# Kernel optimization log

Hardware: AMD Instinct MI355X
Metric: run time of the kernel (lower is better)

The kernel has to match this reference:

```python
import jax, jax.numpy as jnp
import numpy as np

B, S, H, KV, D, HID = 1, 2048, 32, 8, 128, 4096
SCALE = D ** -0.5
EPS = 1e-5
QMAX = 127.0  # 8-bit symmetric fake quant


def fake_quant(x):
    # per-tensor symmetric int8 fake quantization with straight-through estimator
    s = jnp.maximum(jnp.max(jnp.abs(x)), 1e-5) / QMAX
    q = jnp.clip(jnp.round(x / s), -QMAX - 1.0, QMAX) * s
    return x + jax.lax.stop_gradient(q - x)


def rms_norm(x, w):
    xf = x.astype(jnp.float32)
    var = jnp.mean(xf * xf, axis=-1, keepdims=True)
    return (xf * jax.lax.rsqrt(var + EPS)).astype(x.dtype) * w


def rotate_half(x):
    h = x.shape[-1] // 2
    return jnp.concatenate([-x[..., h:], x[..., :h]], axis=-1)


def qlinear(x, W):
    # QuantLinear: fake-quant activation and weight, then matmul (no bias)
    return fake_quant(x) @ fake_quant(W).T


def setup_inputs() -> dict:
    key = jax.random.key(0)
    ks = jax.random.split(key, 5)
    hidden_states = jax.random.normal(ks[0], (B, S, HID), jnp.float32)
    # RoPE tables
    inv_freq = 1.0 / (10000.0 ** (np.arange(0, D, 2, dtype=np.float32) / D))
    freqs = np.outer(np.arange(S, dtype=np.float32), inv_freq)  # [S, D/2]
    emb = np.concatenate([freqs, freqs], axis=-1)  # [S, D]
    cos = jnp.asarray(np.cos(emb))[None]  # [1,S,D]
    sin = jnp.asarray(np.sin(emb))[None]
    # causal additive mask [1,1,S,S]
    mask = jnp.where(np.tril(np.ones((S, S), dtype=bool)), 0.0, -1e9).astype(jnp.float32)[None, None]
    Wq = jax.random.normal(ks[1], (H * D, HID), jnp.float32) * 0.02
    Wk = jax.random.normal(ks[2], (KV * D, HID), jnp.float32) * 0.02
    Wv = jax.random.normal(ks[3], (KV * D, HID), jnp.float32) * 0.02
    Wo = jax.random.normal(ks[4], (HID, H * D), jnp.float32) * 0.02
    q_norm_w = jnp.ones((D,), jnp.float32)
    k_norm_w = jnp.ones((D,), jnp.float32)
    return dict(hidden_states=hidden_states, cos=cos, sin=sin, attention_mask=mask,
                Wq=Wq, Wk=Wk, Wv=Wv, Wo=Wo, q_norm_w=q_norm_w, k_norm_w=k_norm_w)


def reference(hidden_states, cos, sin, attention_mask, Wq, Wk, Wv, Wo, q_norm_w, k_norm_w):
    b, s, _ = hidden_states.shape
    q = qlinear(hidden_states, Wq).reshape(b, s, H, D).transpose(0, 2, 1, 3)   # [B,H,S,D]
    k = qlinear(hidden_states, Wk).reshape(b, s, KV, D).transpose(0, 2, 1, 3)  # [B,KV,S,D]
    v = qlinear(hidden_states, Wv).reshape(b, s, KV, D).transpose(0, 2, 1, 3)
    q = rms_norm(q, q_norm_w)
    k = rms_norm(k, k_norm_w)
    c = cos[:, None]  # unsqueeze head dim -> [1,1,S,D]
    sn = sin[:, None]
    q = q * c + rotate_half(q) * sn
    k = k * c + rotate_half(k) * sn
    n_rep = H // KV
    k = jnp.repeat(k, n_rep, axis=1)  # [B,H,S,D]
    v = jnp.repeat(v, n_rep, axis=1)
    # fake-quant around QK^T
    q = fake_quant(q)
    k = fake_quant(k)
    scores = jnp.einsum('bhqd,bhkd->bhqk', q, k) * SCALE + attention_mask
    p = jax.nn.softmax(scores.astype(jnp.float32), axis=-1).astype(q.dtype)
    # fake-quant around PV
    p = fake_quant(p)
    v = fake_quant(v)
    out = jnp.einsum('bhqk,bhkd->bhqd', p, v)
    out = out.transpose(0, 2, 1, 3).reshape(b, s, H * D)
    return qlinear(out, Wo)
```

## Files before the change

### kernel.cpp

```cpp
#include <hip/hip_runtime.h>
#include <hip/hip_bf16.h>
#include <math.h>
#include <stdint.h>

#define S_LEN 2048
#define NH    32
#define NKV   8
#define HD    128
#define HIDD  4096

typedef unsigned short u16;
typedef __attribute__((ext_vector_type(4))) int i32x4;

#define GLD16(g, l) __builtin_amdgcn_global_load_lds( \
    (const __attribute__((address_space(1))) void*)(g), \
    (__attribute__((address_space(3))) void*)(l), 16, 0, 0)


__device__ __forceinline__ float slot_scale(const unsigned* slot) {
    return fmaxf(__uint_as_float(*slot), 1e-5f) / 127.0f;
}

__device__ __forceinline__ float exp2_fast(float x) {
    float r; asm("v_exp_f32 %0, %1" : "=v"(r) : "v"(x)); return r;
}

__device__ __forceinline__ int qint(float x, float s) {
    float q = rintf(x / s);
    q = fminf(fmaxf(q, -128.0f), 127.0f);
    return (int)q;
}

__device__ __forceinline__ void block_amax_atomic(float m, unsigned* slot) {
    __shared__ float wmax[8];
    const int lane = threadIdx.x & 63;
    const int wid  = threadIdx.x >> 6;
    const int nw   = blockDim.x >> 6;
    #pragma unroll
    for (int o = 32; o; o >>= 1) m = fmaxf(m, __shfl_xor(m, o));
    if (lane == 0) wmax[wid] = m;
    __syncthreads();
    if (threadIdx.x == 0) {
        float bm = wmax[0];
        for (int i = 1; i < nw; ++i) bm = fmaxf(bm, wmax[i]);
        atomicMax(slot, __float_as_uint(bm));
    }
}

struct Amax5Args { const float* p[5]; size_t n4[5]; };
__global__ __launch_bounds__(256) void absmax5_kernel(Amax5Args a, unsigned* slots) {
    const int t = blockIdx.y;
    const float4* x4 = (const float4*)a.p[t];
    const size_t n4 = a.n4[t];
    size_t i = (size_t)blockIdx.x * blockDim.x + threadIdx.x;
    size_t stride = (size_t)gridDim.x * blockDim.x;
    float m = 0.0f;
    for (; i < n4; i += stride) {
        float4 v = x4[i];
        m = fmaxf(m, fmaxf(fmaxf(fabsf(v.x), fabsf(v.y)), fmaxf(fabsf(v.z), fabsf(v.w))));
    }
    block_amax_atomic(m, slots + t);
}

struct Quant5Args { const float* p[5]; char* o[5]; size_t n4[5]; };
__global__ __launch_bounds__(256) void quant5_kernel(Quant5Args a, const unsigned* slots) {
    const int t = blockIdx.y;
    float s = slot_scale(slots + t);
    const float4* x4 = (const float4*)a.p[t];
    unsigned* o4 = (unsigned*)a.o[t];
    const size_t n4 = a.n4[t];
    size_t i = (size_t)blockIdx.x * blockDim.x + threadIdx.x;
    size_t stride = (size_t)gridDim.x * blockDim.x;
    for (; i < n4; i += stride) {
        float4 v = x4[i];
        unsigned o = (unsigned)(qint(v.x, s) & 255)
                   | ((unsigned)(qint(v.y, s) & 255) << 8)
                   | ((unsigned)(qint(v.z, s) & 255) << 16)
                   | ((unsigned)(qint(v.w, s) & 255) << 24);
        o4[i] = o;
    }
}

__global__ __launch_bounds__(256) void quant_kernel(const float* __restrict__ x,
                                                    size_t n4, const unsigned* slot,
                                                    char* __restrict__ out) {
    float s = slot_scale(slot);
    size_t i = (size_t)blockIdx.x * blockDim.x + threadIdx.x;
    size_t stride = (size_t)gridDim.x * blockDim.x;
    const float4* x4 = (const float4*)x;
    unsigned* o4 = (unsigned*)out;
    for (; i < n4; i += stride) {
        float4 v = x4[i];
        unsigned o = (unsigned)(qint(v.x, s) & 255)
                   | ((unsigned)(qint(v.y, s) & 255) << 8)
                   | ((unsigned)(qint(v.z, s) & 255) << 16)
                   | ((unsigned)(qint(v.w, s) & 255) << 24);
        o4[i] = o;
    }
}

__device__ __forceinline__ void gemm_body(const char* __restrict__ A,
                                          const char* __restrict__ B,
                                          float* __restrict__ C,
                                          int m0, int n0, int N, int K,
                                          float scale, unsigned* out_amax,
                                          char* Asm, char* Bsm) {
    const int tid  = threadIdx.x;
    const int lane = tid & 63;
    const int wave = tid >> 6;
    const int wr = (wave >> 1) * 64;
    const int wc = (wave & 1) * 64;
    const int l15 = lane & 15;
    const int l4  = lane >> 4;
    const int cx  = (l4 ^ (l15 & 3)) * 16;
    const int r0  = tid >> 2;
    const int sc  = ((tid & 3) ^ ((tid >> 2) & 3)) * 16;

    i32x4 acc[4][4];
    #pragma unroll
    for (int i = 0; i < 4; ++i)
        #pragma unroll
        for (int j = 0; j < 4; ++j) acc[i][j] = (i32x4){0, 0, 0, 0};

    auto STAGE = [&](int buf, int k0) {
        GLD16(&A[(size_t)(m0 + r0) * K + k0 + sc],      &Asm[buf * 8192 + wave * 1024]);
        GLD16(&A[(size_t)(m0 + 64 + r0) * K + k0 + sc], &Asm[buf * 8192 + 4096 + wave * 1024]);
        GLD16(&B[(size_t)(n0 + r0) * K + k0 + sc],      &Bsm[buf * 8192 + wave * 1024]);
        GLD16(&B[(size_t)(n0 + 64 + r0) * K + k0 + sc], &Bsm[buf * 8192 + 4096 + wave * 1024]);
    };

    STAGE(0, 0);
    __syncthreads();
    int cur = 0;
    const int NT = K >> 6;
    for (int t = 0; t < NT; ++t) {
        if (t + 1 < NT) STAGE(cur ^ 1, (t + 1) << 6);
        i32x4 af[4], bfr[4];
        #pragma unroll
        for (int i = 0; i < 4; ++i)
            af[i] = *(const i32x4*)&Asm[cur * 8192 + (wr + i * 16 + l15) * 64 + cx];
        #pragma unroll
        for (int j = 0; j < 4; ++j)
            bfr[j] = *(const i32x4*)&Bsm[cur * 8192 + (wc + j * 16 + l15) * 64 + cx];
        #pragma unroll
        for (int i = 0; i < 4; ++i)
            #pragma unroll
            for (int j = 0; j < 4; ++j)
                acc[i][j] = __builtin_amdgcn_mfma_i32_16x16x64_i8(af[i], bfr[j], acc[i][j], 0, 0, 0);
        __syncthreads();
        cur ^= 1;
    }

    float lm = 0.0f;
    #pragma unroll
    for (int i = 0; i < 4; ++i)
        #pragma unroll
        for (int j = 0; j < 4; ++j)
            #pragma unroll
            for (int r = 0; r < 4; ++r) {
                int row = m0 + wr + i * 16 + l4 * 4 + r;
                int col = n0 + wc + j * 16 + l15;
                float v = (float)acc[i][j][r] * scale;
                C[(size_t)row * N + col] = v;
                lm = fmaxf(lm, fabsf(v));
            }
    if (out_amax) block_amax_atomic(lm, out_amax);
}

__global__ __launch_bounds__(256) void gemm_qkv_kernel(const char* __restrict__ Aq,
                                                       const char* __restrict__ Wqq,
                                                       const char* __restrict__ Wkq,
                                                       const char* __restrict__ Wvq,
                                                       float* __restrict__ qf,
                                                       float* __restrict__ kf,
                                                       float* __restrict__ vf,
                                                       const unsigned* __restrict__ slots,
                                                       unsigned* v_amax) {
    __shared__ __align__(16) char Asm[2 * 8192];
    __shared__ __align__(16) char Bsm[2 * 8192];
    int bid = blockIdx.x;
    int swz = (bid & 7) * 96 + (bid >> 3);
    int x = swz & 15, y = swz >> 4;
    const char* B; float* C; int N, nb; const unsigned* sB; unsigned* am = nullptr;
    if (y < 32)      { B = Wqq; C = qf; N = NH * HD;  nb = y;      sB = slots + 1; }
    else if (y < 40) { B = Wkq; C = kf; N = NKV * HD; nb = y - 32; sB = slots + 2; }
    else             { B = Wvq; C = vf; N = NKV * HD; nb = y - 40; sB = slots + 3; am = v_amax; }
    float scale = slot_scale(slots + 0) * slot_scale(sB);
    gemm_body(Aq, B, C, x * 128, nb * 128, N, HIDD, scale, am, Asm, Bsm);
}

__global__ __launch_bounds__(256) void gemm_o_kernel(const char* __restrict__ A,
                                                     const char* __restrict__ Woq,
                                                     float* __restrict__ C,
                                                     const unsigned* __restrict__ slots) {
    __shared__ __align__(16) char Asm[2 * 8192];
    __shared__ __align__(16) char Bsm[2 * 8192];
    int bid = blockIdx.x;
    int swz = (bid & 7) * 64 + (bid >> 3);
    int x = swz & 15, y = swz >> 4;
    float scale = slot_scale(slots + 8) * slot_scale(slots + 4);
    gemm_body(A, Woq, C, x * 128, y * 128, NH * HD, HIDD, scale, nullptr, Asm, Bsm);
}

__global__ __launch_bounds__(256) void rmsrope2_kernel(float* __restrict__ qx,
                                                       float* __restrict__ kx,
                                                       const float* __restrict__ cosb,
                                                       const float* __restrict__ sinb,
                                                       const float* __restrict__ qw,
                                                       const float* __restrict__ kw,
                                                       unsigned* slots) {
    const int which = blockIdx.y;
    float* x = which ? kx : qx;
    const float* w = which ? kw : qw;
    const int s_shift = which ? 3 : 5;
    const int nrows = which ? (S_LEN * NKV) : (S_LEN * NH);
    unsigned* slot = slots + (which ? 6 : 5);

    const int lane = threadIdx.x & 63;
    const int wid  = threadIdx.x >> 6;
    const float wa = w[lane];
    const float wb = w[lane + 64];
    float lm = 0.0f;
    for (int row = blockIdx.x * 4 + wid; row < nrows; row += gridDim.x * 4) {
        int s = row >> s_shift;
        float* xr = x + (size_t)row * 128;
        float a = xr[lane], b = xr[lane + 64];
        float ss = a * a + b * b;
        #pragma unroll
        for (int o = 32; o; o >>= 1) ss += __shfl_xor(ss, o);
        float inv = 1.0f / sqrtf(ss * (1.0f / 128.0f) + 1e-5f);
        float ya = (a * inv) * wa;
        float yb = (b * inv) * wb;
        const float* cr = cosb + (size_t)s * 128;
        const float* sr = sinb + (size_t)s * 128;
        float o0 = ya * cr[lane]      - yb * sr[lane];
        float o1 = yb * cr[lane + 64] + ya * sr[lane + 64];
        xr[lane] = o0;
        xr[lane + 64] = o1;
        lm = fmaxf(lm, fmaxf(fabsf(o0), fabsf(o1)));
    }
    block_amax_atomic(lm, slot);
}

__global__ __launch_bounds__(256) void quant_qk2_kernel(const float* __restrict__ qx,
                                                        const float* __restrict__ kx,
                                                        const unsigned* slots,
                                                        char* __restrict__ qq,
                                                        char* __restrict__ kq) {
    int tid = blockIdx.x * 256 + threadIdx.x;
    const int qtot = S_LEN * NH * HD;
    if (tid < qtot) {
        float s = slot_scale(slots + 5);
        int d  = tid & 127;
        int h  = (tid >> 7) & 31;
        int sp = tid >> 12;
        qq[((size_t)h * S_LEN + sp) * 128 + d] = (char)qint(qx[tid], s);
    } else {
        tid -= qtot;
        float s = slot_scale(slots + 6);
        int d  = tid & 127;
        int h  = (tid >> 7) & 7;
        int sp = tid >> 10;
        kq[((size_t)h * S_LEN + sp) * 128 + d] = (char)qint(kx[tid], s);
    }
}

__global__ __launch_bounds__(256) void quant_v_kernel(const float* __restrict__ x,
                                                      const unsigned* slot,
                                                      char* __restrict__ out) {
    __shared__ unsigned char t8[64][36];
    const float s = slot_scale(slot);
    const int t   = threadIdx.x;
    const int sp0 = blockIdx.x * 64;
    const int d0  = blockIdx.y * 32;
    const int kvh = blockIdx.z;
    const int dl = t & 31;
    const int sb = t >> 5;
    #pragma unroll
    for (int j = 0; j < 8; ++j) {
        int spl = sb + j * 8;
        float v = x[((size_t)(sp0 + spl) * NKV + kvh) * 128 + d0 + dl];
        t8[spl][dl] = (unsigned char)qint(v, s);
    }
    __syncthreads();
    const int dd = t >> 3;
    const int ch = t & 7;
    unsigned lo = 0, hi = 0;
    #pragma unroll
    for (int j = 0; j < 4; ++j) lo |= (unsigned)t8[ch * 8 + j][dd] << (8 * j);
    #pragma unroll
    for (int j = 0; j < 4; ++j) hi |= (unsigned)t8[ch * 8 + 4 + j][dd] << (8 * j);
    *(uint2*)&out[((size_t)kvh * 128 + d0 + dd) * S_LEN + sp0 + ch * 8] = make_uint2(lo, hi);
}

__global__ __launch_bounds__(256) void attn_kernel(const char* __restrict__ Qq,
                                                   const char* __restrict__ Kq,
                                                   const char* __restrict__ Vt,
                                                   const unsigned* sq_slot,
                                                   const unsigned* sk_slot,
                                                   const unsigned* sv_slot,
                                                   float* __restrict__ O,
                                                   unsigned* amax_slot) {
    __shared__ __align__(16) char Klds[64 * 144];
    __shared__ __align__(16) char Vlds[128 * 80];
    __shared__ __align__(16) char plds[4][16 * 80];

    const int tid  = threadIdx.x;
    const int lane = tid & 63;
    const int wave = tid >> 6;
    const int h  = blockIdx.y;
    const int kv = h >> 2;
    const int l15 = lane & 15;
    const int l4  = lane >> 4;
    const size_t kvS = (size_t)kv * S_LEN;

    const float sq = slot_scale(sq_slot);
    const float sk = slot_scale(sk_slot);
    const float sv = slot_scale(sv_slot);
    const float qs2 = sq * sk * 0.08838834764831845f * 1.4426950408889634f;
    const float osc = (1.0f / 127.0f) * sv;
    const float NEG = -1e30f;

    float lm = 0.0f;

    #pragma unroll 1
    for (int tpass = 0; tpass < 2; ++tpass) {
        const int qt  = tpass ? (31 - (int)blockIdx.x) : (int)blockIdx.x;
        const int qr0 = qt * 64 + wave * 16;
        const int nchunk = qt + 1;

        i32x4 qf2[2];
        {
            const char* qp = Qq + ((size_t)h * S_LEN + qr0 + l15) * 128 + l4 * 16;
            qf2[0] = *(const i32x4*)(qp);
            qf2[1] = *(const i32x4*)(qp + 64);
        }

        float m_l = NEG, l_l = 0.0f;

        auto qk_block = [&](int hb) -> i32x4 {
            i32x4 sacc = {0, 0, 0, 0};
            #pragma unroll
            for (int c = 0; c < 2; ++c) {
                i32x4 kfa = *(const i32x4*)&Klds[(hb * 16 + l15) * 144 + c * 64 + l4 * 16];
                sacc = __builtin_amdgcn_mfma_i32_16x16x64_i8(kfa, qf2[c], sacc, 0, 0, 0);
            }
            return sacc;
        };
        auto p1_interior = [&](int hb) {
            i32x4 sacc = qk_block(hb);
            float x0 = (float)sacc[0] * qs2, x1 = (float)sacc[1] * qs2;
            float x2 = (float)sacc[2] * qs2, x3 = (float)sacc[3] * qs2;
            float bm = fmaxf(fmaxf(x0, x1), fmaxf(x2, x3));
            float mn = fmaxf(m_l, bm);
            float ps = exp2_fast(x0 - mn) + exp2_fast(x1 - mn)
                     + exp2_fast(x2 - mn) + exp2_fast(x3 - mn);
            l_l = l_l * exp2_fast(m_l - mn) + ps;
            m_l = mn;
        };
        auto p1_diag = [&](int hb) {
            i32x4 sacc = qk_block(hb);
            float x[4];
            #pragma unroll
            for (int r = 0; r < 4; ++r) {
                float v = (float)sacc[r] * qs2;
                x[r] = ((l4 * 4 + r) > l15) ? NEG : v;
            }
            float bm = fmaxf(fmaxf(x[0], x[1]), fmaxf(x[2], x[3]));
            float mn = fmaxf(m_l, bm);
            float ps = exp2_fast(x[0] - mn) + exp2_fast(x[1] - mn)
                     + exp2_fast(x[2] - mn) + exp2_fast(x[3] - mn);
            l_l = l_l * exp2_fast(m_l - mn) + ps;
            m_l = mn;
        };

        i32x4 kreg[2];
        #pragma unroll
        for (int c = 0; c < 2; ++c) {
            int idx = c * 256 + tid;
            kreg[c] = *(const i32x4*)&Kq[(kvS + (idx >> 3)) * 128 + (idx & 7) * 16];
        }
        #pragma unroll 1
        for (int kc = 0; kc < nchunk; ++kc) {
            __syncthreads();
            #pragma unroll
            for (int c = 0; c < 2; ++c) {
                int idx = c * 256 + tid;
                *(i32x4*)&Klds[(idx >> 3) * 144 + (idx & 7) * 16] = kreg[c];
            }
            __syncthreads();
            if (kc + 1 < nchunk) {
                #pragma unroll
                for (int c = 0; c < 2; ++c) {
                    int idx = c * 256 + tid;
                    kreg[c] = *(const i32x4*)&Kq[(kvS + (kc + 1) * 64 + (idx >> 3)) * 128 + (idx & 7) * 16];
                }
            }
            if (kc < qt) {
                p1_interior(0); p1_interior(1); p1_interior(2); p1_interior(3);
            } else {
                #pragma unroll
                for (int hb = 0; hb < 4; ++hb) {
                    if (hb < wave) p1_interior(hb);
                    else if (hb == wave) p1_diag(hb);
                }
            }
        }
        float m2 = fmaxf(m_l, __shfl_xor(m_l, 16));
        float mfin = fmaxf(m2, __shfl_xor(m2, 32));
        float t = l_l * exp2_fast(m_l - mfin);
        t += __shfl_xor(t, 16);
        t += __shfl_xor(t, 32);
        float rl = 127.0f / t;

        i32x4 oacc[8];
        #pragma unroll
        for (int dt = 0; dt < 8; ++dt) oacc[dt] = (i32x4){0, 0, 0, 0};

        auto p2_interior = [&](int hb) -> unsigned {
            i32x4 sacc = qk_block(hb);
            unsigned pack = 0;
            #pragma unroll
            for (int r = 0; r < 4; ++r) {
                float x = (float)sacc[r] * qs2;
                float pq = rintf(exp2_fast(x - mfin) * rl);
                pack |= ((unsigned)(int)pq) << (8 * r);
            }
            return pack;
        };
        auto p2_diag = [&](int hb) -> unsigned {
            i32x4 sacc = qk_block(hb);
            unsigned pack = 0;
            #pragma unroll
            for (int r = 0; r < 4; ++r) {
                float x = (float)sacc[r] * qs2;
                float p = exp2_fast(x - mfin) * rl;
                float pq = ((l4 * 4 + r) > l15) ? 0.0f : rintf(p);
                pack |= ((unsigned)(int)pq) << (8 * r);
            }
            return pack;
        };

        i32x4 vreg[2];
        #pragma unroll
        for (int c = 0; c < 2; ++c) {
            int idx = c * 256 + tid;
            kreg[c] = *(const i32x4*)&Kq[(kvS + (idx >> 3)) * 128 + (idx & 7) * 16];
            vreg[c] = *(const i32x4*)&Vt[((size_t)kv * 128 + (idx >> 2)) * S_LEN + (idx & 3) * 16];
        }
        #pragma unroll 1
        for (int kc = 0; kc < nchunk; ++kc) {
            __syncthreads();
            #pragma unroll
            for (int c = 0; c < 2; ++c) {
                int idx = c * 256 + tid;
                *(i32x4*)&Klds[(idx >> 3) * 144 + (idx & 7) * 16] = kreg[c];
                *(i32x4*)&Vlds[(idx >> 2) * 80 + (idx & 3) * 16] = vreg[c];
            }
            __syncthreads();
            if (kc + 1 < nchunk) {
                #pragma unroll
                for (int c = 0; c < 2; ++c) {
                    int idx = c * 256 + tid;
                    kreg[c] = *(const i32x4*)&Kq[(kvS + (kc + 1) * 64 + (idx >> 3)) * 128 + (idx & 7) * 16];
                    vreg[c] = *(const i32x4*)&Vt[((size_t)kv * 128 + (idx >> 2)) * S_LEN + (kc + 1) * 64 + (idx & 3) * 16];
                }
            }
            if (kc < qt) {
                #pragma unroll
                for (int hb = 0; hb < 4; ++hb)
                    *(unsigned*)&plds[wave][l15 * 80 + hb * 16 + l4 * 4] = p2_interior(hb);
            } else {
                #pragma unroll
                for (int hb = 0; hb < 4; ++hb) {
                    unsigned pack = 0;
                    if (hb < wave) pack = p2_interior(hb);
                    else if (hb == wave) pack = p2_diag(hb);
                    *(unsigned*)&plds[wave][l15 * 80 + hb * 16 + l4 * 4] = pack;
                }
            }
            i32x4 pf = *(const i32x4*)&plds[wave][l15 * 80 + l4 * 16];
            #pragma unroll
            for (int dt = 0; dt < 8; ++dt) {
                i32x4 vfb = *(const i32x4*)&Vlds[(dt * 16 + l15) * 80 + l4 * 16];
                oacc[dt] = __builtin_amdgcn_mfma_i32_16x16x64_i8(pf, vfb, oacc[dt], 0, 0, 0);
            }
        }

        #pragma unroll
        for (int dt = 0; dt < 8; ++dt)
            #pragma unroll
            for (int r = 0; r < 4; ++r) {
                int qrow = qr0 + l4 * 4 + r;
                float v = (float)oacc[dt][r] * osc;
                O[(size_t)qrow * (NH * 128) + h * 128 + dt * 16 + l15] = v;
                lm = fmaxf(lm, fabsf(v));
            }
    }
    block_amax_atomic(lm, amax_slot);
}

extern "C" void kernel_launch(void* const* d_in, const int* in_sizes, int n_in,
                              void* d_out, int out_size, void* d_ws, size_t ws_size,
                              hipStream_t stream) {
    const float* hs   = (const float*)d_in[0];
    const float* cosb = (const float*)d_in[1];
    const float* sinb = (const float*)d_in[2];
    const float* Wq   = (const float*)d_in[4];
    const float* Wk   = (const float*)d_in[5];
    const float* Wv   = (const float*)d_in[6];
    const float* Wo   = (const float*)d_in[7];
    const float* qnw  = (const float*)d_in[8];
    const float* knw  = (const float*)d_in[9];
    float* out = (float*)d_out;

    char* ws = (char*)d_ws;
    unsigned* slots = (unsigned*)ws;
    size_t off = 256;
    auto take = [&](size_t bytes) { size_t o = off; off += (bytes + 255) & ~(size_t)255; return o; };
    char*  hsq  = (char*)(ws + take((size_t)S_LEN * HIDD));
    char*  Wqq  = (char*)(ws + take((size_t)NH * HD * HIDD));
    char*  Wkq  = (char*)(ws + take((size_t)NKV * HD * HIDD));
    char*  Wvq  = (char*)(ws + take((size_t)NKV * HD * HIDD));
    char*  Woq  = (char*)(ws + take((size_t)HIDD * NH * HD));
    float* qf   = (float*)(ws + take((size_t)S_LEN * NH * HD * 4));
    float* kf   = (float*)(ws + take((size_t)S_LEN * NKV * HD * 4));
    float* vf   = (float*)(ws + take((size_t)S_LEN * NKV * HD * 4));
    char*  qq   = (char*)(ws + take((size_t)NH * S_LEN * HD));
    char*  kq   = (char*)(ws + take((size_t)NKV * S_LEN * HD));
    char*  vtq  = (char*)(ws + take((size_t)NKV * HD * S_LEN));
    float* attnf = qf;
    char*  attnq = hsq;

    hipMemsetAsync(ws, 0, 64, stream);

    const size_t n_hs = (size_t)S_LEN * HIDD;
    const size_t n_wq = (size_t)NH * HD * HIDD;
    const size_t n_wk = (size_t)NKV * HD * HIDD;

    Amax5Args aa;
    aa.p[0] = hs; aa.p[1] = Wq; aa.p[2] = Wk; aa.p[3] = Wv; aa.p[4] = Wo;
    aa.n4[0] = n_hs / 4; aa.n4[1] = n_wq / 4; aa.n4[2] = n_wk / 4;
    aa.n4[3] = n_wk / 4; aa.n4[4] = n_wq / 4;
    absmax5_kernel<<<dim3(512, 5), 256, 0, stream>>>(aa, slots);

    Quant5Args qa;
    qa.p[0] = hs; qa.p[1] = Wq; qa.p[2] = Wk; qa.p[3] = Wv; qa.p[4] = Wo;
    qa.o[0] = hsq; qa.o[1] = Wqq; qa.o[2] = Wkq; qa.o[3] = Wvq; qa.o[4] = Woq;
    qa.n4[0] = n_hs / 4; qa.n4[1] = n_wq / 4; qa.n4[2] = n_wk / 4;
    qa.n4[3] = n_wk / 4; qa.n4[4] = n_wq / 4;
    quant5_kernel<<<dim3(1024, 5), 256, 0, stream>>>(qa, slots);

    gemm_qkv_kernel<<<768, 256, 0, stream>>>(hsq, Wqq, Wkq, Wvq, qf, kf, vf,
                                             slots, slots + 7);

    rmsrope2_kernel<<<dim3(1024, 2), 256, 0, stream>>>(qf, kf, cosb, sinb, qnw, knw, slots);

    quant_qk2_kernel<<<40960, 256, 0, stream>>>(qf, kf, slots, qq, kq);
    quant_v_kernel<<<dim3(32, 4, 8), 256, 0, stream>>>(vf, slots + 7, vtq);

    attn_kernel<<<dim3(16, NH), 256, 0, stream>>>(qq, kq, vtq,
                                                  slots + 5, slots + 6, slots + 7,
                                                  attnf, slots + 8);

    quant_kernel<<<2048, 256, 0, stream>>>(attnf, n_hs / 4, slots + 8, attnq);
    gemm_o_kernel<<<512, 256, 0, stream>>>(attnq, Woq, out, slots);
    (void)in_sizes; (void)n_in; (void)out_size; (void)ws_size;
}
```

Before: 361.2 us.

## Fuse paired causal query tiles into one K/V sweep per block

```diff
diff --git a/kernel.cpp b/kernel.cpp
--- a/kernel.cpp
+++ b/kernel.cpp
@@ -23,6 +23,9 @@
 
 __device__ __forceinline__ float exp2_fast(float x) {
     float r; asm("v_exp_f32 %0, %1" : "=v"(r) : "v"(x)); return r;
+}
+__device__ __forceinline__ float log2_fast(float x) {
+    float r; asm("v_log_f32 %0, %1" : "=v"(r) : "v"(x)); return r;
 }
 
 __device__ __forceinline__ int qint(float x, float s) {
@@ -303,7 +306,8 @@
                                                    unsigned* amax_slot) {
     __shared__ __align__(16) char Klds[64 * 144];
     __shared__ __align__(16) char Vlds[128 * 80];
-    __shared__ __align__(16) char plds[4][16 * 80];
+    __shared__ __align__(16) char pldsB[4][16 * 80];
+    __shared__ __align__(16) char pldsS[4][16 * 80];
 
     const int tid  = threadIdx.x;
     const int lane = tid & 63;
@@ -314,6 +318,11 @@
     const int l4  = lane >> 4;
     const size_t kvS = (size_t)kv * S_LEN;
 
+    const int qtS = blockIdx.x;
+    const int qtB = 31 - qtS;
+    const int qr0S = qtS * 64 + wave * 16;
+    const int qr0B = qtB * 64 + wave * 16;
+
     const float sq = slot_scale(sq_slot);
     const float sk = slot_scale(sk_slot);
     const float sv = slot_scale(sv_slot);
@@ -321,182 +330,213 @@
     const float osc = (1.0f / 127.0f) * sv;
     const float NEG = -1e30f;
 
-    float lm = 0.0f;
-
+    i32x4 qfS[2], qfB[2];
+    {
+        const char* qpS = Qq + ((size_t)h * S_LEN + qr0S + l15) * 128 + l4 * 16;
+        const char* qpB = Qq + ((size_t)h * S_LEN + qr0B + l15) * 128 + l4 * 16;
+        qfS[0] = *(const i32x4*)(qpS); qfS[1] = *(const i32x4*)(qpS + 64);
+        qfB[0] = *(const i32x4*)(qpB); qfB[1] = *(const i32x4*)(qpB + 64);
+    }
+
+    auto qk_block = [&](int hb, const i32x4* qf2) -> i32x4 {
+        i32x4 sacc = {0, 0, 0, 0};
+        #pragma unroll
+        for (int c = 0; c < 2; ++c) {
+            i32x4 kfa = *(const i32x4*)&Klds[(hb * 16 + l15) * 144 + c * 64 + l4 * 16];
+            sacc = __builtin_amdgcn_mfma_i32_16x16x64_i8(kfa, qf2[c], sacc, 0, 0, 0);
+        }
+        return sacc;
+    };
+
+    float mS = NEG, lS = 0.0f, mB = NEG, lB = 0.0f;
+
+    auto p1_interior = [&](int hb, const i32x4* qf2, float& m_l, float& l_l) {
+        i32x4 sacc = qk_block(hb, qf2);
+        float x0 = (float)sacc[0] * qs2, x1 = (float)sacc[1] * qs2;
+        float x2 = (float)sacc[2] * qs2, x3 = (float)sacc[3] * qs2;
+        float bm = fmaxf(fmaxf(x0, x1), fmaxf(x2, x3));
+        float mn = fmaxf(m_l, bm);
+        float ps = exp2_fast(x0 - mn) + exp2_fast(x1 - mn)
+                 + exp2_fast(x2 - mn) + exp2_fast(x3 - mn);
+        l_l = l_l * exp2_fast(m_l - mn) + ps;
+        m_l = mn;
+    };
+    auto p1_diag = [&](int hb, const i32x4* qf2, float& m_l, float& l_l) {
+        i32x4 sacc = qk_block(hb, qf2);
+        float x[4];
+        #pragma unroll
+        for (int r = 0; r < 4; ++r) {
+            float v = (float)sacc[r] * qs2;
+            x[r] = ((l4 * 4 + r) > l15) ? NEG : v;
+        }
+        float bm = fmaxf(fmaxf(x[0], x[1]), fmaxf(x[2], x[3]));
+        float mn = fmaxf(m_l, bm);
+        float ps = exp2_fast(x[0] - mn) + exp2_fast(x[1] - mn)
+                 + exp2_fast(x[2] - mn) + exp2_fast(x[3] - mn);
+        l_l = l_l * exp2_fast(m_l - mn) + ps;
+        m_l = mn;
+    };
+
+    i32x4 kreg[2];
+    #pragma unroll
+    for (int c = 0; c < 2; ++c) {
+        int idx = c * 256 + tid;
+        kreg[c] = *(const i32x4*)&Kq[(kvS + (idx >> 3)) * 128 + (idx & 7) * 16];
+    }
     #pragma unroll 1
-    for (int tpass = 0; tpass < 2; ++tpass) {
-        const int qt  = tpass ? (31 - (int)blockIdx.x) : (int)blockIdx.x;
-        const int qr0 = qt * 64 + wave * 16;
-        const int nchunk = qt + 1;
-
-        i32x4 qf2[2];
-        {
-            const char* qp = Qq + ((size_t)h * S_LEN + qr0 + l15) * 128 + l4 * 16;
-            qf2[0] = *(const i32x4*)(qp);
-            qf2[1] = *(const i32x4*)(qp + 64);
-        }
-
-        float m_l = NEG, l_l = 0.0f;
-
-        auto qk_block = [&](int hb) -> i32x4 {
-            i32x4 sacc = {0, 0, 0, 0};
-            #pragma unroll
-            for (int c = 0; c < 2; ++c) {
-                i32x4 kfa = *(const i32x4*)&Klds[(hb * 16 + l15) * 144 + c * 64 + l4 * 16];
-                sacc = __builtin_amdgcn_mfma_i32_16x16x64_i8(kfa, qf2[c], sacc, 0, 0, 0);
-            }
-            return sacc;
-        };
-        auto p1_interior = [&](int hb) {
-            i32x4 sacc = qk_block(hb);
-            float x0 = (float)sacc[0] * qs2, x1 = (float)sacc[1] * qs2;
-            float x2 = (float)sacc[2] * qs2, x3 = (float)sacc[3] * qs2;
-            float bm = fmaxf(fmaxf(x0, x1), fmaxf(x2, x3));
-            float mn = fmaxf(m_l, bm);
-            float ps = exp2_fast(x0 - mn) + exp2_fast(x1 - mn)
-                     + exp2_fast(x2 - mn) + exp2_fast(x3 - mn);
-            l_l = l_l * exp2_fast(m_l - mn) + ps;
-            m_l = mn;
-        };
-        auto p1_diag = [&](int hb) {
-            i32x4 sacc = qk_block(hb);
-            float x[4];
-            #pragma unroll
-            for (int r = 0; r < 4; ++r) {
-                float v = (float)sacc[r] * qs2;
-                x[r] = ((l4 * 4 + r) > l15) ? NEG : v;
-            }
-            float bm = fmaxf(fmaxf(x[0], x[1]), fmaxf(x[2], x[3]));
-            float mn = fmaxf(m_l, bm);
-            float ps = exp2_fast(x[0] - mn) + exp2_fast(x[1] - mn)
-                     + exp2_fast(x[2] - mn) + exp2_fast(x[3] - mn);
-            l_l = l_l * exp2_fast(m_l - mn) + ps;
-            m_l = mn;
-        };
-
-        i32x4 kreg[2];
+    for (int kc = 0; kc <= qtB; ++kc) {
+        __syncthreads();
         #pragma unroll
         for (int c = 0; c < 2; ++c) {
             int idx = c * 256 + tid;
-            kreg[c] = *(const i32x4*)&Kq[(kvS + (idx >> 3)) * 128 + (idx & 7) * 16];
-        }
-        #pragma unroll 1
-        for (int kc = 0; kc < nchunk; ++kc) {
-            __syncthreads();
+            *(i32x4*)&Klds[(idx >> 3) * 144 + (idx & 7) * 16] = kreg[c];
+        }
+        __syncthreads();
+        if (kc < qtB) {
             #pragma unroll
             for (int c = 0; c < 2; ++c) {
                 int idx = c * 256 + tid;
-                *(i32x4*)&Klds[(idx >> 3) * 144 + (idx & 7) * 16] = kreg[c];
+                kreg[c] = *(const i32x4*)&Kq[(kvS + (kc + 1) * 64 + (idx >> 3)) * 128 + (idx & 7) * 16];
             }
-            __syncthreads();
-            if (kc + 1 < nchunk) {
-                #pragma unroll
-                for (int c = 0; c < 2; ++c) {
-                    int idx = c * 256 + tid;
-                    kreg[c] = *(const i32x4*)&Kq[(kvS + (kc + 1) * 64 + (idx >> 3)) * 128 + (idx & 7) * 16];
-                }
+        }
+        if (kc < qtB) {
+            p1_interior(0, qfB, mB, lB); p1_interior(1, qfB, mB, lB);
+            p1_interior(2, qfB, mB, lB); p1_interior(3, qfB, mB, lB);
+        } else {
+            #pragma unroll
+            for (int hb = 0; hb < 4; ++hb) {
+                if (hb < wave) p1_interior(hb, qfB, mB, lB);
+                else if (hb == wave) p1_diag(hb, qfB, mB, lB);
             }
-            if (kc < qt) {
-                p1_interior(0); p1_interior(1); p1_interior(2); p1_interior(3);
-            } else {
-                #pragma unroll
-                for (int hb = 0; hb < 4; ++hb) {
-                    if (hb < wave) p1_interior(hb);
-                    else if (hb == wave) p1_diag(hb);
-                }
+        }
+        if (kc < qtS) {
+            p1_interior(0, qfS, mS, lS); p1_interior(1, qfS, mS, lS);
+            p1_interior(2, qfS, mS, lS); p1_interior(3, qfS, mS, lS);
+        } else if (kc == qtS) {
+            #pragma unroll
+            for (int hb = 0; hb < 4; ++hb) {
+                if (hb < wave) p1_interior(hb, qfS, mS, lS);
+                else if (hb == wave) p1_diag(hb, qfS, mS, lS);
             }
         }
+    }
+    auto merge = [&](float m_l, float l_l) -> float2 {
         float m2 = fmaxf(m_l, __shfl_xor(m_l, 16));
         float mfin = fmaxf(m2, __shfl_xor(m2, 32));
         float t = l_l * exp2_fast(m_l - mfin);
         t += __shfl_xor(t, 16);
         t += __shfl_xor(t, 32);
-        float rl = 127.0f / t;
-
-        i32x4 oacc[8];
-        #pragma unroll
-        for (int dt = 0; dt < 8; ++dt) oacc[dt] = (i32x4){0, 0, 0, 0};
-
-        auto p2_interior = [&](int hb) -> unsigned {
-            i32x4 sacc = qk_block(hb);
-            unsigned pack = 0;
-            #pragma unroll
-            for (int r = 0; r < 4; ++r) {
-                float x = (float)sacc[r] * qs2;
-                float pq = rintf(exp2_fast(x - mfin) * rl);
-                pack |= ((unsigned)(int)pq) << (8 * r);
-            }
-            return pack;
-        };
-        auto p2_diag = [&](int hb) -> unsigned {
-            i32x4 sacc = qk_block(hb);
-            unsigned pack = 0;
-            #pragma unroll
-            for (int r = 0; r < 4; ++r) {
-                float x = (float)sacc[r] * qs2;
-                float p = exp2_fast(x - mfin) * rl;
-                float pq = ((l4 * 4 + r) > l15) ? 0.0f : rintf(p);
-                pack |= ((unsigned)(int)pq) << (8 * r);
-            }
-            return pack;
-        };
-
-        i32x4 vreg[2];
+        return make_float2(mfin, mfin - log2_fast(127.0f / t));
+    };
+    float2 mcS = merge(mS, lS);
+    float2 mcB = merge(mB, lB);
+    const float cS = mcS.y, cB = mcB.y;
+
+    i32x4 oaccS[8], oaccB[8];
+    #pragma unroll
+    for (int dt = 0; dt < 8; ++dt) {
+        oaccS[dt] = (i32x4){0, 0, 0, 0};
+        oaccB[dt] = (i32x4){0, 0, 0, 0};
+    }
+
+    auto p2_interior = [&](int hb, const i32x4* qf2, float c) -> unsigned {
+        i32x4 sacc = qk_block(hb, qf2);
+        unsigned pack = 0;
+        #pragma unroll
+        for (int r = 0; r < 4; ++r) {
+            float pq = rintf(exp2_fast((float)sacc[r] * qs2 - c));
+            pack |= ((unsigned)(int)pq) << (8 * r);
+        }
+        return pack;
+    };
+    auto p2_diag = [&](int hb, const i32x4* qf2, float c) -> unsigned {
+        i32x4 sacc = qk_block(hb, qf2);
+        unsigned pack = 0;
+        #pragma unroll
+        for (int r = 0; r < 4; ++r) {
+            float p = exp2_fast((float)sacc[r] * qs2 - c);
+            float pq = ((l4 * 4 + r) > l15) ? 0.0f : rintf(p);
+            pack |= ((unsigned)(int)pq) << (8 * r);
+        }
+        return pack;
+    };
+    auto pv8 = [&](char (*plds)[16 * 80], i32x4* oacc) {
+        i32x4 pf = *(const i32x4*)&plds[wave][l15 * 80 + l4 * 16];
+        #pragma unroll
+        for (int dt = 0; dt < 8; ++dt) {
+            i32x4 vfb = *(const i32x4*)&Vlds[(dt * 16 + l15) * 80 + l4 * 16];
+            oacc[dt] = __builtin_amdgcn_mfma_i32_16x16x64_i8(pf, vfb, oacc[dt], 0, 0, 0);
+        }
+    };
+
+    i32x4 vreg[2];
+    #pragma unroll
+    for (int c = 0; c < 2; ++c) {
+        int idx = c * 256 + tid;
+        kreg[c] = *(const i32x4*)&Kq[(kvS + (idx >> 3)) * 128 + (idx & 7) * 16];
+        vreg[c] = *(const i32x4*)&Vt[((size_t)kv * 128 + (idx >> 2)) * S_LEN + (idx & 3) * 16];
+    }
+    #pragma unroll 1
+    for (int kc = 0; kc <= qtB; ++kc) {
+        __syncthreads();
         #pragma unroll
         for (int c = 0; c < 2; ++c) {
             int idx = c * 256 + tid;
-            kreg[c] = *(const i32x4*)&Kq[(kvS + (idx >> 3)) * 128 + (idx & 7) * 16];
-            vreg[c] = *(const i32x4*)&Vt[((size_t)kv * 128 + (idx >> 2)) * S_LEN + (idx & 3) * 16];
-        }
-        #pragma unroll 1
-        for (int kc = 0; kc < nchunk; ++kc) {
-            __syncthreads();
+            *(i32x4*)&Klds[(idx >> 3) * 144 + (idx & 7) * 16] = kreg[c];
+            *(i32x4*)&Vlds[(idx >> 2) * 80 + (idx & 3) * 16] = vreg[c];
+        }
+        __syncthreads();
+        if (kc < qtB) {
             #pragma unroll
             for (int c = 0; c < 2; ++c) {
                 int idx = c * 256 + tid;
-                *(i32x4*)&Klds[(idx >> 3) * 144 + (idx & 7) * 16] = kreg[c];
-                *(i32x4*)&Vlds[(idx >> 2) * 80 + (idx & 3) * 16] = vreg[c];
+                kreg[c] = *(const i32x4*)&Kq[(kvS + (kc + 1) * 64 + (idx >> 3)) * 128 + (idx & 7) * 16];
+                vreg[c] = *(const i32x4*)&Vt[((size_t)kv * 128 + (idx >> 2)) * S_LEN + (kc + 1) * 64 + (idx & 3) * 16];
             }
-            __syncthreads();
-            if (kc + 1 < nchunk) {
-                #pragma unroll
-                for (int c = 0; c < 2; ++c) {
-                    int idx = c * 256 + tid;
-                    kreg[c] = *(const i32x4*)&Kq[(kvS + (kc + 1) * 64 + (idx >> 3)) * 128 + (idx & 7) * 16];
-                    vreg[c] = *(const i32x4*)&Vt[((size_t)kv * 128 + (idx >> 2)) * S_LEN + (kc + 1) * 64 + (idx & 3) * 16];
-                }
+        }
+        if (kc < qtB) {
+            #pragma unroll
+            for (int hb = 0; hb < 4; ++hb)
+                *(unsigned*)&pldsB[wave][l15 * 80 + hb * 16 + l4 * 4] = p2_interior(hb, qfB, cB);
+        } else {
+            #pragma unroll
+            for (int hb = 0; hb < 4; ++hb) {
+                unsigned pack = 0;
+                if (hb < wave) pack = p2_interior(hb, qfB, cB);
+                else if (hb == wave) pack = p2_diag(hb, qfB, cB);
+                *(unsigned*)&pldsB[wave][l15 * 80 + hb * 16 + l4 * 4] = pack;
             }
-            if (kc < qt) {
-                #pragma unroll
-                for (int hb = 0; hb < 4; ++hb)
-                    *(unsigned*)&plds[wave][l15 * 80 + hb * 16 + l4 * 4] = p2_interior(hb);
-            } else {
-                #pragma unroll
-                for (int hb = 0; hb < 4; ++hb) {
-                    unsigned pack = 0;
-                    if (hb < wave) pack = p2_interior(hb);
-                    else if (hb == wave) pack = p2_diag(hb);
-                    *(unsigned*)&plds[wave][l15 * 80 + hb * 16 + l4 * 4] = pack;
-                }
+        }
+        pv8(pldsB, oaccB);
+        if (kc < qtS) {
+            #pragma unroll
+            for (int hb = 0; hb < 4; ++hb)
+                *(unsigned*)&pldsS[wave][l15 * 80 + hb * 16 + l4 * 4] = p2_interior(hb, qfS, cS);
+            pv8(pldsS, oaccS);
+        } else if (kc == qtS) {
+            #pragma unroll
+            for (int hb = 0; hb < 4; ++hb) {
+                unsigned pack = 0;
+                if (hb < wave) pack = p2_interior(hb, qfS, cS);
+                else if (hb == wave) pack = p2_diag(hb, qfS, cS);
+                *(unsigned*)&pldsS[wave][l15 * 80 + hb * 16 + l4 * 4] = pack;
             }
-            i32x4 pf = *(const i32x4*)&plds[wave][l15 * 80 + l4 * 16];
-            #pragma unroll
-            for (int dt = 0; dt < 8; ++dt) {
-                i32x4 vfb = *(const i32x4*)&Vlds[(dt * 16 + l15) * 80 + l4 * 16];
-                oacc[dt] = __builtin_amdgcn_mfma_i32_16x16x64_i8(pf, vfb, oacc[dt], 0, 0, 0);
-            }
-        }
-
-        #pragma unroll
-        for (int dt = 0; dt < 8; ++dt)
-            #pragma unroll
-            for (int r = 0; r < 4; ++r) {
-                int qrow = qr0 + l4 * 4 + r;
-                float v = (float)oacc[dt][r] * osc;
-                O[(size_t)qrow * (NH * 128) + h * 128 + dt * 16 + l15] = v;
-                lm = fmaxf(lm, fabsf(v));
-            }
-    }
+            pv8(pldsS, oaccS);
+        }
+    }
+
+    float lm = 0.0f;
+    #pragma unroll
+    for (int dt = 0; dt < 8; ++dt)
+        #pragma unroll
+        for (int r = 0; r < 4; ++r) {
+            float vB = (float)oaccB[dt][r] * osc;
+            float vS = (float)oaccS[dt][r] * osc;
+            int col = h * 128 + dt * 16 + l15;
+            O[(size_t)(qr0B + l4 * 4 + r) * (NH * 128) + col] = vB;
+            O[(size_t)(qr0S + l4 * 4 + r) * (NH * 128) + col] = vS;
+            lm = fmaxf(lm, fmaxf(fabsf(vB), fabsf(vS)));
+        }
     block_amax_atomic(lm, amax_slot);
 }
 
```

Result: no change. 363.1 us (+0.5%).
